# Kernel tuning notes

Hardware: AMD Instinct MI355X
Metric: run time of the kernel (lower is better)

## Reference

```python
import jax, jax.numpy as jnp
import numpy as np
from jax import lax

STRIDE = 2
PADDING = 2
KSIZE = 5


def _maxpool3d(y, k):
    # valid max pool with kernel=stride=k over the 3 spatial dims of NCDHW
    return lax.reduce_window(
        y, -jnp.inf, lax.max,
        window_dimensions=(1, 1, k, k, k),
        window_strides=(1, 1, k, k, k),
        padding='VALID')


def setup_inputs() -> dict:
    key = jax.random.key(0)
    k1, k2, k3 = jax.random.split(key, 3)
    x = jax.random.normal(k1, (16, 32, 16, 32, 32), dtype=jnp.float32)
    # torch ConvTranspose3d weight layout: (in_ch, out_ch, kD, kH, kW)
    weight = jax.random.normal(k2, (32, 64, KSIZE, KSIZE, KSIZE), dtype=jnp.float32) * 0.05
    bias = jax.random.normal(k3, (64,), dtype=jnp.float32) * 0.05
    return {"x": x, "weight": weight, "bias": bias}


def reference(x, weight, bias):
    # Fused ConvTranspose3d + sum over output channels.
    # sum_c convT(x, W)[:, c] == convT(x, W.sum(out_ch)) + bias.sum(), so we
    # pre-reduce the weight over the out-channel axis (axis=1) -- same math,
    # and it never materializes the (N, out_ch, D', H', W') intermediate,
    # exactly like the fused CUDA kernel.
    w_sum = weight.sum(axis=1)  # (in_ch, kD, kH, kW)
    # transposed conv == conv with lhs_dilation=stride, pad k-1-p, flipped kernel
    wk = w_sum[None, :, ::-1, ::-1, ::-1]  # (1, in_ch, kD, kH, kW), OIDHW
    pad = KSIZE - 1 - PADDING
    y = lax.conv_general_dilated(
        x, wk,
        window_strides=(1, 1, 1),
        padding=[(pad, pad)] * 3,
        lhs_dilation=(STRIDE, STRIDE, STRIDE),
        dimension_numbers=('NCDHW', 'OIDHW', 'NCDHW'))  # (N,1,31,63,63)
    y = y + bias.sum()
    # MaxPool3d(kernel=2) then MaxPool3d(kernel=3) on the single-channel map
    y = _maxpool3d(y, 2)  # (N,1,15,31,31)
    y = _maxpool3d(y, 3)  # (N,1,5,10,10)
    return y
```

## Files before the change

### kernel.cpp

```cpp
#include <hip/hip_runtime.h>


typedef short v8s __attribute__((ext_vector_type(8)));
typedef float v4f __attribute__((ext_vector_type(4)));
typedef unsigned short ushort_t;

#define DIN 16
#define HIN 32
#define WIN 32
#define CHSTR (DIN*HIN*WIN)
#define NSTRIDE (32*CHSTR)
#define Y_N 108000
#define Y_TOT (16*Y_N)
#define XSTR 24

#define XT_US 10653696u
#define XTN   665856u
#define PLANE_US 36992u
#define ROW_US 1088u
#define BT_BYTE_OFF 21307392u
#define WSF_BYTE_OFF 21335040u
#define NEED_MFMA (21335040u + 4097u*4u)

static __device__ __forceinline__ ushort_t f2bf(float f) {
  unsigned u = __builtin_bit_cast(unsigned, f);
  unsigned r = (u + 0x7FFFu + ((u >> 16) & 1u)) >> 16;
  return (ushort_t)r;
}

__global__ __launch_bounds__(256) void transpose_x(const float* __restrict__ x,
                                                   const float* __restrict__ w,
                                                   const float* __restrict__ bias,
                                                   ushort_t* __restrict__ xT,
                                                   ushort_t* __restrict__ Btab,
                                                   float* __restrict__ wsf) {
  int blk = blockIdx.x;
  int t = threadIdx.x;

  if (blk >= 1088) {
    int abc = blk - 1088;
    int a = abc / 9, b = (abc / 3) % 3, c = abc % 3;
    int half = t & 3;
    int l = t >> 2;
    int tt = l & 15, g = l >> 4;
    float v0 = 0.f, v1 = 0.f;
    if (tt < 8) {
      int td = tt & 1, th = (tt >> 1) & 1, tw = tt >> 2;
      int kd = td + 2 * a, kh = th + 2 * b, kw = tw + 2 * c;
      if (kd < 5 && kh < 5 && kw < 5) {
        int off = kd * 25 + kh * 5 + kw;
        const float* wp0 = w + (size_t)(8 * g + 2 * half) * 64 * 125 + off;
        const float* wp1 = wp0 + 64 * 125;
        float s0 = 0.f, s1 = 0.f;
#pragma unroll
        for (int oc = 0; oc < 64; ++oc) { s0 += wp0[oc * 125]; s1 += wp1[oc * 125]; }
        v0 = s0; v1 = s1;
      }
    }
    unsigned pk = (unsigned)f2bf(v0) | ((unsigned)f2bf(v1) << 16);
    ((unsigned*)Btab)[(abc * 64 + l) * 4 + half] = pk;
    if (abc == 0 && t == 0) {
      float bsum = 0.f;
      for (int o = 0; o < 64; ++o) bsum += bias[o];
      wsf[4096] = bsum;
    }
    return;
  }

  int hq = blk & 3;
  int dpad = (blk >> 2) % 17;
  int n = blk / 68;
  int h0 = 8 * hq;
  ushort_t* plane = xT + (size_t)(n * 18 + dpad) * PLANE_US;
  int d = dpad - 1;

  if (d < 0) {
    for (int r = 0; r < 8; ++r) {
      char* row = (char*)(plane + (size_t)(h0 + r) * ROW_US);
      for (int s = t; s < 136; s += 256)
        *(uint4*)(row + s * 16) = make_uint4(0, 0, 0, 0);
    }
    return;
  }

  __shared__ float lb[2][32 * 33];
  const float* xb = x + ((size_t)n * 32 * 16 + d) * 1024;
  int ic = t >> 3, wq = t & 7;

  {
    int h = h0 - 1;
    if (h >= 0) {
      float4 v = *(const float4*)&xb[(size_t)ic * 16384 + h * 32 + wq * 4];
      float* L = lb[0] + ic * 33 + wq * 4;
      L[0] = v.x; L[1] = v.y; L[2] = v.z; L[3] = v.w;
    }
  }
  int pp = 0;
  for (int i = 0; i < 8; ++i) {
    __syncthreads();
    if (i + 1 < 8) {
      int h = h0 + i;
      if (h <= 31) {
        float4 v = *(const float4*)&xb[(size_t)ic * 16384 + h * 32 + wq * 4];
        float* L = lb[pp ^ 1] + ic * 33 + wq * 4;
        L[0] = v.x; L[1] = v.y; L[2] = v.z; L[3] = v.w;
      }
    }
    int h = h0 + i - 1;
    ushort_t* row = plane + (size_t)(h0 + i) * ROW_US;
    bool hv = (h >= 0 && h <= 31);
    for (int s = t; s < 136; s += 256) {
      int wslot = s >> 2, q4 = s & 3;
      ushort_t o[8];
#pragma unroll
      for (int j = 0; j < 8; ++j) o[j] = 0;
      if (wslot >= 1 && wslot <= 32 && hv) {
        int w2 = wslot - 1;
        const float* L = lb[pp];
#pragma unroll
        for (int j = 0; j < 8; ++j) o[j] = f2bf(L[(8 * q4 + j) * 33 + w2]);
      }
      uint4 pk;
      pk.x = (unsigned)o[0] | ((unsigned)o[1] << 16);
      pk.y = (unsigned)o[2] | ((unsigned)o[3] << 16);
      pk.z = (unsigned)o[4] | ((unsigned)o[5] << 16);
      pk.w = (unsigned)o[6] | ((unsigned)o[7] << 16);
      *(uint4*)(row + wslot * 32 + q4 * 8) = pk;
    }
    pp ^= 1;
  }
}

__global__ __launch_bounds__(576, 7) void conv_mfma(const ushort_t* __restrict__ xT,
                                                    const ushort_t* __restrict__ Btab,
                                                    const float* __restrict__ wsf,
                                                    float* __restrict__ out) {
  __shared__ __align__(16) ushort_t As0[5440];
  __shared__ __align__(16) ushort_t As1[5440];
  __shared__ float ytile[6 * 6 * 64];
  __shared__ float red[64];

  int blk = blockIdx.x;
  int OH = blk % 10, OD = (blk / 10) % 5, n = blk / 50;
  int t = threadIdx.x;

  int wv = t >> 6, l = t & 63;
  int mdl = wv / 3, mhl = wv % 3;
  int tt = l & 15, g = l >> 4;
  const ushort_t* xn = xT + (size_t)n * XTN;
  const ushort_t* slab0 = xn + ((size_t)(3 * OD) * 34 + 3 * OH) * ROW_US;

  {
    uint4 v0 = *(const uint4*)(slab0 + t * 8);
    uint4 v1;
    if (t < 104) v1 = *(const uint4*)(slab0 + (t + 576) * 8);
    *(uint4*)&As0[t * 8] = v0;
    if (t < 104) *(uint4*)&As0[(t + 576) * 8] = v1;
  }
  __syncthreads();

  v4f acc0 = {0.f, 0.f, 0.f, 0.f};
  v4f acc1 = {0.f, 0.f, 0.f, 0.f};
  int lane_off = tt * 32 + g * 8;

  for (int p = 0; p < 5; ++p) {
    uint4 v0, v1;
    if (p < 4) {
      const ushort_t* slab = slab0 + (size_t)(p + 1) * 34 * ROW_US;
      v0 = *(const uint4*)(slab + t * 8);
      if (t < 104) v1 = *(const uint4*)(slab + (t + 576) * 8);
    }

    int a = mdl + 2 - p;
    if (0 <= a && a <= 2) {
      const ushort_t* Ab = (p & 1) ? As1 : As0;
      const ushort_t* Bg = Btab + ((size_t)a * 9 * 64 + l) * 8;
#pragma unroll
      for (int b = 0; b < 3; ++b) {
#pragma unroll
        for (int c = 0; c < 3; ++c) {
          int idx = ((mhl + 2 - b) * 34 + (2 - c)) * 32 + lane_off;
          v8s bv = *(const v8s*)(Bg + (b * 3 + c) * 512);
          v8s a0 = *(const v8s*)&Ab[idx];
          v8s a1 = *(const v8s*)&Ab[idx + 512];
          acc0 = __builtin_amdgcn_mfma_f32_16x16x32_bf16(a0, bv, acc0, 0, 0, 0);
          acc1 = __builtin_amdgcn_mfma_f32_16x16x32_bf16(a1, bv, acc1, 0, 0, 0);
        }
      }
    }

    if (p < 4) {
      ushort_t* dst = (p & 1) ? As0 : As1;
      *(uint4*)&dst[t * 8] = v0;
      if (t < 104) *(uint4*)&dst[(t + 576) * 8] = v1;
      __syncthreads();
    }
  }

  __syncthreads();
  if (tt < 8) {
    int td = tt & 1, th = (tt >> 1) & 1, tw = tt >> 2;
    int odl = 2 * mdl + td, ohl = 2 * mhl + th;
#pragma unroll
    for (int i = 0; i < 4; ++i) {
      int mwD0 = 4 * g + i;
      ytile[(odl * 6 + ohl) * 64 + 2 * mwD0 + tw] = acc0[i];
      ytile[(odl * 6 + ohl) * 64 + 2 * (16 + mwD0) + tw] = acc1[i];
    }
  }
  __syncthreads();

  if (t < 60) {
    int odl = t / 10, OW = t % 10;
    float m = -3.4e38f;
    for (int oh = 0; oh < 6; ++oh)
#pragma unroll
      for (int j = 0; j < 6; ++j)
        m = fmaxf(m, ytile[(odl * 6 + oh) * 64 + 6 * OW + j]);
    red[t] = m;
  }
  __syncthreads();
  if (t < 10) {
    float m = red[t];
#pragma unroll
    for (int odl = 1; odl < 6; ++odl) m = fmaxf(m, red[odl * 10 + t]);
    out[((n * 5 + OD) * 10 + OH) * 10 + t] = m + wsf[4096];
  }
}

template<int NCHUNK>
__global__ __launch_bounds__(256, 4) void conv_stage1(const float* __restrict__ x,
                                                      const float* __restrict__ ws,
                                                      float* part, int woff) {
  constexpr int ICPB = 32 / NCHUNK;
  constexpr int NPHS = ICPB / 2;
  __shared__ __align__(16) float xs[170 * XSTR];
  int blk = blockIdx.x;
  int s0 = blk % 320;
  int chunk = blk / 320;
  int wq = s0 & 1, hq = (s0 >> 1) & 1, dc = (s0 >> 2) % 5, n = s0 / 20;
  int t = threadIdx.x;
  int mw = t % 15, lmh = t / 15;
  int id_base = 3 * dc - 1, ih_base = 15 * hq - 1;
  int iwb = wq ? 12 : -4;
  int cb = mw + (wq ? 2 : 3);
  const float* xn = x + (size_t)n * NSTRIDE + (size_t)(chunk * ICPB) * CHSTR;
  const float* wsw = ws + woff + (size_t)(chunk * ICPB) * 128;
  float acc[3][2][2][2] = {{{{0.f}}}};
  for (int phs = 0; phs < NPHS; ++phs) {
    for (int s = t; s < 1700; s += 256) {
      int c2 = s % 10, row = s / 10;
      int bh = row % 17, q = row / 17;
      int ad = q % 5, lic = q / 5;
      int id = id_base + ad, ih = ih_base + bh, iw = iwb + 2 * c2;
      float2 v = make_float2(0.f, 0.f);
      if ((id | ih | iw) >= 0)
        v = *(const float2*)&xn[(size_t)(phs * 2 + lic) * CHSTR + (id * HIN + ih) * WIN + iw];
      *(float2*)&xs[row * XSTR + 2 * c2] = v;
    }
    __syncthreads();
    if (t < 225) {
#pragma unroll
      for (int lic = 0; lic < 2; ++lic) {
        const float* wc = wsw + (size_t)(phs * 2 + lic) * 128;
        const float* xc = &xs[(lic * 85 + lmh) * XSTR + cb];
        float xv[5][3][3];
#pragma unroll
        for (int a = 0; a < 5; ++a)
#pragma unroll
          for (int b = 0; b < 3; ++b) {
            const float* xr = xc + (a * 17 + b) * XSTR;
            xv[a][b][0] = xr[0]; xv[a][b][1] = xr[1]; xv[a][b][2] = xr[2];
          }
#pragma unroll
        for (int kd = 0; kd < 5; ++kd) {
          constexpr int DT[5] = {0, 1, 0, 1, 0};
          constexpr int AOFF[5] = {2, 2, 1, 1, 0};
          const int dt = DT[kd], aoff = AOFF[kd];
          float wv[25];
#pragma unroll
          for (int j = 0; j < 25; ++j) wv[j] = wc[kd * 25 + j];
#pragma unroll
          for (int kh = 0; kh < 5; ++kh) {
            constexpr int HT[5] = {0, 1, 0, 1, 0};
            constexpr int BOFF[5] = {2, 2, 1, 1, 0};
            const int ht = HT[kh], boff = BOFF[kh];
#pragma unroll
            for (int m = 0; m < 3; ++m) {
              const float x0 = xv[m + aoff][boff][0];
              const float x1 = xv[m + aoff][boff][1];
              const float x2 = xv[m + aoff][boff][2];
              acc[m][dt][ht][0] += x0 * wv[kh * 5 + 4];
              acc[m][dt][ht][0] += x1 * wv[kh * 5 + 2];
              acc[m][dt][ht][0] += x2 * wv[kh * 5 + 0];
              acc[m][dt][ht][1] += x1 * wv[kh * 5 + 3];
              acc[m][dt][ht][1] += x2 * wv[kh * 5 + 1];
            }
          }
        }
      }
    }
    __syncthreads();
  }
  if (t < 225) {
    float* pb = part + (size_t)chunk * Y_TOT + (size_t)n * Y_N;
#pragma unroll
    for (int m = 0; m < 3; ++m)
#pragma unroll
      for (int dt = 0; dt < 2; ++dt)
#pragma unroll
        for (int ht = 0; ht < 2; ++ht) {
          int od_g = 6 * dc + 2 * m + dt;
          int oh_g = 30 * hq + 2 * lmh + ht;
          int ow_g = 30 * wq + 2 * mw;
          *(float2*)&pb[(od_g * 60 + oh_g) * 60 + ow_g] =
              make_float2(acc[m][dt][ht][0], acc[m][dt][ht][1]);
        }
  }
}

template<int NCHUNK>
__global__ __launch_bounds__(256) void pool_stage2(const float* __restrict__ part,
                                                   const float* __restrict__ ws,
                                                   float* __restrict__ out, int woff) {
  __shared__ __align__(16) float buf[2160];
  __shared__ float red[240];
  int blk = blockIdx.x;
  int hc = blk % 10, dc = (blk / 10) % 5, n = blk / 50;
  int t = threadIdx.x;
  const float* pb = part + (size_t)n * Y_N;
  for (int s = t; s < 540; s += 256) {
    int row = s / 15, c4 = s % 15;
    int od = row / 6, oh = row % 6;
    size_t idx = (size_t)((6 * dc + od) * 60 + (6 * hc + oh)) * 60 + 4 * c4;
    float4 v = *(const float4*)&pb[idx];
#pragma unroll
    for (int c = 1; c < NCHUNK; ++c) {
      float4 u = *(const float4*)&pb[(size_t)c * Y_TOT + idx];
      v.x += u.x; v.y += u.y; v.z += u.z; v.w += u.w;
    }
    *(float4*)&buf[row * 60 + 4 * c4] = v;
  }
  __syncthreads();
  if (t < 240) {
    int wc = t / 24, sub = t % 24;
    float m = -3.4e38f;
#pragma unroll
    for (int k = 0; k < 9; ++k) {
      int e = sub + 24 * k;
      int od = e / 36, r = e % 36;
      int oh = r / 6, ow0 = r % 6;
      m = fmaxf(m, buf[(od * 6 + oh) * 60 + 6 * wc + ow0]);
    }
    red[t] = m;
  }
  __syncthreads();
  if (t < 10) {
    float mm = -3.4e38f;
#pragma unroll
    for (int s2 = 0; s2 < 24; ++s2) mm = fmaxf(mm, red[t * 24 + s2]);
    out[((n * 5 + dc) * 10 + hc) * 10 + t] = mm + ws[woff + 4096];
  }
}

__global__ __launch_bounds__(128) void prep2(const float* __restrict__ w,
                                             const float* __restrict__ bias,
                                             float* __restrict__ ws, int woff) {
  int i = blockIdx.x, t = threadIdx.x;
  if (t < 125) {
    const float* wp = w + (size_t)i * 64 * 125 + t;
    float v = 0.f;
#pragma unroll
    for (int o = 0; o < 64; ++o) v += wp[o * 125];
    ws[woff + i * 128 + t] = v;
  }
  if (i == 0 && t == 126) {
    float b = 0.f;
    for (int o = 0; o < 64; ++o) b += bias[o];
    ws[woff + 4096] = b;
  }
}

extern "C" void kernel_launch(void* const* d_in, const int* in_sizes, int n_in,
                              void* d_out, int out_size, void* d_ws, size_t ws_size,
                              hipStream_t stream) {
  const float* x    = (const float*)d_in[0];
  const float* w    = (const float*)d_in[1];
  const float* bias = (const float*)d_in[2];
  float* outp = (float*)d_out;

  if (ws_size >= (size_t)NEED_MFMA) {
    ushort_t* xT = (ushort_t*)d_ws;
    ushort_t* Bt = (ushort_t*)((char*)d_ws + BT_BYTE_OFF);
    float* wsf   = (float*)((char*)d_ws + WSF_BYTE_OFF);
    transpose_x<<<1088 + 27, 256, 0, stream>>>(x, w, bias, xT, Bt, wsf);
    conv_mfma<<<800, 576, 0, stream>>>(xT, Bt, wsf, outp);
    return;
  }

  float* ws = (float*)d_ws;
  const size_t need4 = ((size_t)4 * Y_TOT + 4097) * 4;
  const size_t need2 = ((size_t)2 * Y_TOT + 4097) * 4;
  const size_t need1 = ((size_t)1 * Y_TOT + 4097) * 4;
  if (ws_size >= need4) {
    int woff = 4 * Y_TOT;
    prep2<<<32, 128, 0, stream>>>(w, bias, ws, woff);
    conv_stage1<4><<<320 * 4, 256, 0, stream>>>(x, ws, ws, woff);
    pool_stage2<4><<<800, 256, 0, stream>>>(ws, ws, outp, woff);
  } else if (ws_size >= need2) {
    int woff = 2 * Y_TOT;
    prep2<<<32, 128, 0, stream>>>(w, bias, ws, woff);
    conv_stage1<2><<<320 * 2, 256, 0, stream>>>(x, ws, ws, woff);
    pool_stage2<2><<<800, 256, 0, stream>>>(ws, ws, outp, woff);
  } else if (ws_size >= need1) {
    int woff = 1 * Y_TOT;
    prep2<<<32, 128, 0, stream>>>(w, bias, ws, woff);
    conv_stage1<1><<<320 * 1, 256, 0, stream>>>(x, ws, ws, woff);
    pool_stage2<1><<<800, 256, 0, stream>>>(ws, ws, outp, woff);
  }
}
```

Before: 36.08 us.

## Fuse x transpose/bf16 conversion into MFMA conv kernel, drop intermediate xT buffer

Removes the separate transpose_x pass that wrote a padded bf16 copy of x to global memory. The conv kernel now loads fp32 x directly, converts it to bf16 and stores it into a swizzled LDS layout, with padding zeroed in-kernel. This drops a global write and read of about 21MB and shrinks the preceding launch to a small weight-prep kernel. In exchange, each block does strided fp32 gathers across channels (8 loads per thread, 32 lanes wide) and reloads halo data, which may coalesce worse. The fallback paths are also simplified to a single chunk.

Result: slower. 39.60 us (+9.8%).

```diff
diff --git a/kernel.cpp b/kernel.cpp
--- a/kernel.cpp
+++ b/kernel.cpp
@@ -5,136 +5,60 @@
 typedef float v4f __attribute__((ext_vector_type(4)));
 typedef unsigned short ushort_t;
 
-#define DIN 16
-#define HIN 32
-#define WIN 32
-#define CHSTR (DIN*HIN*WIN)
+#define CHSTR 16384
 #define NSTRIDE (32*CHSTR)
 #define Y_N 108000
 #define Y_TOT (16*Y_N)
 #define XSTR 24
 
-#define XT_US 10653696u
-#define XTN   665856u
-#define PLANE_US 36992u
-#define ROW_US 1088u
-#define BT_BYTE_OFF 21307392u
-#define WSF_BYTE_OFF 21335040u
-#define NEED_MFMA (21335040u + 4097u*4u)
+#define WSF_BYTE_OFF 27648u
+#define NEED_FUSED (27648u + 4097u*4u)
 
 static __device__ __forceinline__ ushort_t f2bf(float f) {
   unsigned u = __builtin_bit_cast(unsigned, f);
   unsigned r = (u + 0x7FFFu + ((u >> 16) & 1u)) >> 16;
   return (ushort_t)r;
 }
-
-__global__ __launch_bounds__(256) void transpose_x(const float* __restrict__ x,
-                                                   const float* __restrict__ w,
-                                                   const float* __restrict__ bias,
-                                                   ushort_t* __restrict__ xT,
-                                                   ushort_t* __restrict__ Btab,
-                                                   float* __restrict__ wsf) {
-  int blk = blockIdx.x;
+static __device__ __forceinline__ unsigned pk2(float a, float b) {
+  return (unsigned)f2bf(a) | ((unsigned)f2bf(b) << 16);
+}
+
+__global__ __launch_bounds__(256) void prep_bw(const float* __restrict__ w,
+                                               const float* __restrict__ bias,
+                                               ushort_t* __restrict__ Btab,
+                                               float* __restrict__ wsf) {
+  int abc = blockIdx.x;
+  int a = abc / 9, b = (abc / 3) % 3, c = abc % 3;
   int t = threadIdx.x;
-
-  if (blk >= 1088) {
-    int abc = blk - 1088;
-    int a = abc / 9, b = (abc / 3) % 3, c = abc % 3;
-    int half = t & 3;
-    int l = t >> 2;
-    int tt = l & 15, g = l >> 4;
-    float v0 = 0.f, v1 = 0.f;
-    if (tt < 8) {
-      int td = tt & 1, th = (tt >> 1) & 1, tw = tt >> 2;
-      int kd = td + 2 * a, kh = th + 2 * b, kw = tw + 2 * c;
-      if (kd < 5 && kh < 5 && kw < 5) {
-        int off = kd * 25 + kh * 5 + kw;
-        const float* wp0 = w + (size_t)(8 * g + 2 * half) * 64 * 125 + off;
-        const float* wp1 = wp0 + 64 * 125;
-        float s0 = 0.f, s1 = 0.f;
-#pragma unroll
-        for (int oc = 0; oc < 64; ++oc) { s0 += wp0[oc * 125]; s1 += wp1[oc * 125]; }
-        v0 = s0; v1 = s1;
-      }
-    }
-    unsigned pk = (unsigned)f2bf(v0) | ((unsigned)f2bf(v1) << 16);
-    ((unsigned*)Btab)[(abc * 64 + l) * 4 + half] = pk;
-    if (abc == 0 && t == 0) {
-      float bsum = 0.f;
-      for (int o = 0; o < 64; ++o) bsum += bias[o];
-      wsf[4096] = bsum;
-    }
-    return;
-  }
-
-  int hq = blk & 3;
-  int dpad = (blk >> 2) % 17;
-  int n = blk / 68;
-  int h0 = 8 * hq;
-  ushort_t* plane = xT + (size_t)(n * 18 + dpad) * PLANE_US;
-  int d = dpad - 1;
-
-  if (d < 0) {
-    for (int r = 0; r < 8; ++r) {
-      char* row = (char*)(plane + (size_t)(h0 + r) * ROW_US);
-      for (int s = t; s < 136; s += 256)
-        *(uint4*)(row + s * 16) = make_uint4(0, 0, 0, 0);
-    }
-    return;
-  }
-
-  __shared__ float lb[2][32 * 33];
-  const float* xb = x + ((size_t)n * 32 * 16 + d) * 1024;
-  int ic = t >> 3, wq = t & 7;
-
-  {
-    int h = h0 - 1;
-    if (h >= 0) {
-      float4 v = *(const float4*)&xb[(size_t)ic * 16384 + h * 32 + wq * 4];
-      float* L = lb[0] + ic * 33 + wq * 4;
-      L[0] = v.x; L[1] = v.y; L[2] = v.z; L[3] = v.w;
-    }
-  }
-  int pp = 0;
-  for (int i = 0; i < 8; ++i) {
-    __syncthreads();
-    if (i + 1 < 8) {
-      int h = h0 + i;
-      if (h <= 31) {
-        float4 v = *(const float4*)&xb[(size_t)ic * 16384 + h * 32 + wq * 4];
-        float* L = lb[pp ^ 1] + ic * 33 + wq * 4;
-        L[0] = v.x; L[1] = v.y; L[2] = v.z; L[3] = v.w;
-      }
-    }
-    int h = h0 + i - 1;
-    ushort_t* row = plane + (size_t)(h0 + i) * ROW_US;
-    bool hv = (h >= 0 && h <= 31);
-    for (int s = t; s < 136; s += 256) {
-      int wslot = s >> 2, q4 = s & 3;
-      ushort_t o[8];
-#pragma unroll
-      for (int j = 0; j < 8; ++j) o[j] = 0;
-      if (wslot >= 1 && wslot <= 32 && hv) {
-        int w2 = wslot - 1;
-        const float* L = lb[pp];
-#pragma unroll
-        for (int j = 0; j < 8; ++j) o[j] = f2bf(L[(8 * q4 + j) * 33 + w2]);
-      }
-      uint4 pk;
-      pk.x = (unsigned)o[0] | ((unsigned)o[1] << 16);
-      pk.y = (unsigned)o[2] | ((unsigned)o[3] << 16);
-      pk.z = (unsigned)o[4] | ((unsigned)o[5] << 16);
-      pk.w = (unsigned)o[6] | ((unsigned)o[7] << 16);
-      *(uint4*)(row + wslot * 32 + q4 * 8) = pk;
-    }
-    pp ^= 1;
-  }
-}
-
-__global__ __launch_bounds__(576, 7) void conv_mfma(const ushort_t* __restrict__ xT,
-                                                    const ushort_t* __restrict__ Btab,
-                                                    const float* __restrict__ wsf,
-                                                    float* __restrict__ out) {
+  int half = t & 3;
+  int l = t >> 2;
+  int tt = l & 15, g = l >> 4;
+  float v0 = 0.f, v1 = 0.f;
+  if (tt < 8) {
+    int td = tt & 1, th = (tt >> 1) & 1, tw = tt >> 2;
+    int kd = td + 2 * a, kh = th + 2 * b, kw = tw + 2 * c;
+    if (kd < 5 && kh < 5 && kw < 5) {
+      int off = kd * 25 + kh * 5 + kw;
+      const float* wp0 = w + (size_t)(8 * g + 2 * half) * 64 * 125 + off;
+      const float* wp1 = wp0 + 64 * 125;
+      float s0 = 0.f, s1 = 0.f;
+#pragma unroll
+      for (int oc = 0; oc < 64; ++oc) { s0 += wp0[oc * 125]; s1 += wp1[oc * 125]; }
+      v0 = s0; v1 = s1;
+    }
+  }
+  ((unsigned*)Btab)[(abc * 64 + l) * 4 + half] = (unsigned)f2bf(v0) | ((unsigned)f2bf(v1) << 16);
+  if (abc == 0 && t == 0) {
+    float bs = 0.f;
+    for (int o = 0; o < 64; ++o) bs += bias[o];
+    wsf[4096] = bs;
+  }
+}
+
+__global__ __launch_bounds__(576, 7) void conv_fused(const float* __restrict__ x,
+                                                     const ushort_t* __restrict__ Btab,
+                                                     const float* __restrict__ wsf,
+                                                     float* __restrict__ out) {
   __shared__ __align__(16) ushort_t As0[5440];
   __shared__ __align__(16) ushort_t As1[5440];
   __shared__ float ytile[6 * 6 * 64];
@@ -143,46 +67,86 @@
   int blk = blockIdx.x;
   int OH = blk % 10, OD = (blk / 10) % 5, n = blk / 50;
   int t = threadIdx.x;
-
   int wv = t >> 6, l = t & 63;
   int mdl = wv / 3, mhl = wv % 3;
   int tt = l & 15, g = l >> 4;
-  const ushort_t* xn = xT + (size_t)n * XTN;
-  const ushort_t* slab0 = xn + ((size_t)(3 * OD) * 34 + 3 * OH) * ROW_US;
+
+  int sw = l & 31, sich = l >> 5;
+  int wcol = sw + 1;
+  int r_u = wv >> 1, icg_u = wv & 1;
+  bool hz_u = (3 * OH + r_u) == 0;
+  const float* xu = x + (size_t)(n * 32 + icg_u * 16 + sich * 8) * CHSTR
+                      + (3 * OH + r_u - 1) * 32 + sw;
+  int waddr_u = ((r_u * 34 + wcol) << 5) + (((icg_u * 2 + sich) ^ (wcol & 3)) << 3);
+  const float* xu9 = x + (size_t)(n * 32 + 16 + sich * 8) * CHSTR + (3 * OH + 3) * 32 + sw;
+  int waddr_9 = ((4 * 34 + wcol) << 5) + (((2 + sich) ^ (wcol & 3)) << 3);
+
+  int oc0 = ((2 + tt) << 5) + ((g ^ ((tt + 2) & 3)) << 3);
+  int oc1 = ((1 + tt) << 5) + ((g ^ ((tt + 1) & 3)) << 3);
+  int oc2 = ((tt) << 5)     + ((g ^ (tt & 3)) << 3);
 
   {
-    uint4 v0 = *(const uint4*)(slab0 + t * 8);
-    uint4 v1;
-    if (t < 104) v1 = *(const uint4*)(slab0 + (t + 576) * 8);
-    *(uint4*)&As0[t * 8] = v0;
-    if (t < 104) *(uint4*)&As0[(t + 576) * 8] = v1;
+    float f[8];
+#pragma unroll
+    for (int j = 0; j < 8; ++j) f[j] = 0.f;
+    if (OD != 0 && !hz_u) {
+      const float* s = xu + (size_t)(3 * OD - 1) * 1024;
+#pragma unroll
+      for (int j = 0; j < 8; ++j) f[j] = s[(size_t)j * CHSTR];
+    }
+    uint4 pk;
+    pk.x = pk2(f[0], f[1]); pk.y = pk2(f[2], f[3]);
+    pk.z = pk2(f[4], f[5]); pk.w = pk2(f[6], f[7]);
+    *(uint4*)&As0[waddr_u] = pk;
+    if (wv == 8) {
+      float f9[8];
+#pragma unroll
+      for (int j = 0; j < 8; ++j) f9[j] = 0.f;
+      if (OD != 0) {
+        const float* s = xu9 + (size_t)(3 * OD - 1) * 1024;
+#pragma unroll
+        for (int j = 0; j < 8; ++j) f9[j] = s[(size_t)j * CHSTR];
+      }
+      uint4 p9;
+      p9.x = pk2(f9[0], f9[1]); p9.y = pk2(f9[2], f9[3]);
+      p9.z = pk2(f9[4], f9[5]); p9.w = pk2(f9[6], f9[7]);
+      *(uint4*)&As0[waddr_9] = p9;
+    }
+    if (t < 160) {
+      int seg = t >> 4;
+      int rr = seg >> 1, col = (seg & 1) ? 33 : 0;
+      *(unsigned*)&As0[((rr * 34 + col) << 5) + ((t & 15) << 1)] = 0u;
+    }
   }
   __syncthreads();
 
   v4f acc0 = {0.f, 0.f, 0.f, 0.f};
   v4f acc1 = {0.f, 0.f, 0.f, 0.f};
-  int lane_off = tt * 32 + g * 8;
 
   for (int p = 0; p < 5; ++p) {
-    uint4 v0, v1;
-    if (p < 4) {
-      const ushort_t* slab = slab0 + (size_t)(p + 1) * 34 * ROW_US;
-      v0 = *(const uint4*)(slab + t * 8);
-      if (t < 104) v1 = *(const uint4*)(slab + (t + 576) * 8);
+    float pf[8];
+#pragma unroll
+    for (int j = 0; j < 8; ++j) pf[j] = 0.f;
+    if (p < 4 && !hz_u) {
+      const float* s = xu + (size_t)(3 * OD + p) * 1024;
+#pragma unroll
+      for (int j = 0; j < 8; ++j) pf[j] = s[(size_t)j * CHSTR];
     }
 
     int a = mdl + 2 - p;
     if (0 <= a && a <= 2) {
       const ushort_t* Ab = (p & 1) ? As1 : As0;
-      const ushort_t* Bg = Btab + ((size_t)a * 9 * 64 + l) * 8;
+      const ushort_t* Bg = Btab + ((size_t)(a * 9) * 64 + l) * 8;
 #pragma unroll
       for (int b = 0; b < 3; ++b) {
+        int rb = (mhl + 2 - b) * 1088;
 #pragma unroll
         for (int c = 0; c < 3; ++c) {
-          int idx = ((mhl + 2 - b) * 34 + (2 - c)) * 32 + lane_off;
+          int offc = (c == 0) ? oc0 : (c == 1) ? oc1 : oc2;
           v8s bv = *(const v8s*)(Bg + (b * 3 + c) * 512);
-          v8s a0 = *(const v8s*)&Ab[idx];
-          v8s a1 = *(const v8s*)&Ab[idx + 512];
+          const ushort_t* ap = Ab + rb + offc;
+          v8s a0 = *(const v8s*)ap;
+          v8s a1 = *(const v8s*)(ap + 512);
           acc0 = __builtin_amdgcn_mfma_f32_16x16x32_bf16(a0, bv, acc0, 0, 0, 0);
           acc1 = __builtin_amdgcn_mfma_f32_16x16x32_bf16(a1, bv, acc1, 0, 0, 0);
         }
@@ -191,8 +155,25 @@
 
     if (p < 4) {
       ushort_t* dst = (p & 1) ? As0 : As1;
-      *(uint4*)&dst[t * 8] = v0;
-      if (t < 104) *(uint4*)&dst[(t + 576) * 8] = v1;
+      uint4 pk;
+      pk.x = pk2(pf[0], pf[1]); pk.y = pk2(pf[2], pf[3]);
+      pk.z = pk2(pf[4], pf[5]); pk.w = pk2(pf[6], pf[7]);
+      *(uint4*)&dst[waddr_u] = pk;
+      if (wv == 8) {
+        float f9[8];
+        const float* s = xu9 + (size_t)(3 * OD + p) * 1024;
+#pragma unroll
+        for (int j = 0; j < 8; ++j) f9[j] = s[(size_t)j * CHSTR];
+        uint4 p9;
+        p9.x = pk2(f9[0], f9[1]); p9.y = pk2(f9[2], f9[3]);
+        p9.z = pk2(f9[4], f9[5]); p9.w = pk2(f9[6], f9[7]);
+        *(uint4*)&dst[waddr_9] = p9;
+      }
+      if (p == 0 && t < 160) {
+        int seg = t >> 4;
+        int rr = seg >> 1, col = (seg & 1) ? 33 : 0;
+        *(unsigned*)&dst[((rr * 34 + col) << 5) + ((t & 15) << 1)] = 0u;
+      }
       __syncthreads();
     }
   }
@@ -228,26 +209,40 @@
   }
 }
 
-template<int NCHUNK>
+__global__ __launch_bounds__(128) void prep2(const float* __restrict__ w,
+                                             const float* __restrict__ bias,
+                                             float* __restrict__ ws, int woff) {
+  int i = blockIdx.x, t = threadIdx.x;
+  if (t < 125) {
+    const float* wp = w + (size_t)i * 64 * 125 + t;
+    float v = 0.f;
+#pragma unroll
+    for (int o = 0; o < 64; ++o) v += wp[o * 125];
+    ws[woff + i * 128 + t] = v;
+  }
+  if (i == 0 && t == 126) {
+    float b = 0.f;
+    for (int o = 0; o < 64; ++o) b += bias[o];
+    ws[woff + 4096] = b;
+  }
+}
+
 __global__ __launch_bounds__(256, 4) void conv_stage1(const float* __restrict__ x,
                                                       const float* __restrict__ ws,
                                                       float* part, int woff) {
-  constexpr int ICPB = 32 / NCHUNK;
-  constexpr int NPHS = ICPB / 2;
   __shared__ __align__(16) float xs[170 * XSTR];
   int blk = blockIdx.x;
   int s0 = blk % 320;
-  int chunk = blk / 320;
   int wq = s0 & 1, hq = (s0 >> 1) & 1, dc = (s0 >> 2) % 5, n = s0 / 20;
   int t = threadIdx.x;
   int mw = t % 15, lmh = t / 15;
   int id_base = 3 * dc - 1, ih_base = 15 * hq - 1;
   int iwb = wq ? 12 : -4;
   int cb = mw + (wq ? 2 : 3);
-  const float* xn = x + (size_t)n * NSTRIDE + (size_t)(chunk * ICPB) * CHSTR;
-  const float* wsw = ws + woff + (size_t)(chunk * ICPB) * 128;
+  const float* xn = x + (size_t)n * NSTRIDE;
+  const float* wsw = ws + woff;
   float acc[3][2][2][2] = {{{{0.f}}}};
-  for (int phs = 0; phs < NPHS; ++phs) {
+  for (int phs = 0; phs < 16; ++phs) {
     for (int s = t; s < 1700; s += 256) {
       int c2 = s % 10, row = s / 10;
       int bh = row % 17, q = row / 17;
@@ -255,7 +250,7 @@
       int id = id_base + ad, ih = ih_base + bh, iw = iwb + 2 * c2;
       float2 v = make_float2(0.f, 0.f);
       if ((id | ih | iw) >= 0)
-        v = *(const float2*)&xn[(size_t)(phs * 2 + lic) * CHSTR + (id * HIN + ih) * WIN + iw];
+        v = *(const float2*)&xn[(size_t)(phs * 2 + lic) * CHSTR + (id * 32 + ih) * 32 + iw];
       *(float2*)&xs[row * XSTR + 2 * c2] = v;
     }
     __syncthreads();
@@ -277,9 +272,9 @@
           constexpr int DT[5] = {0, 1, 0, 1, 0};
           constexpr int AOFF[5] = {2, 2, 1, 1, 0};
           const int dt = DT[kd], aoff = AOFF[kd];
-          float wv[25];
-#pragma unroll
-          for (int j = 0; j < 25; ++j) wv[j] = wc[kd * 25 + j];
+          float wvv[25];
+#pragma unroll
+          for (int j = 0; j < 25; ++j) wvv[j] = wc[kd * 25 + j];
 #pragma unroll
           for (int kh = 0; kh < 5; ++kh) {
             constexpr int HT[5] = {0, 1, 0, 1, 0};
@@ -290,11 +285,11 @@
               const float x0 = xv[m + aoff][boff][0];
               const float x1 = xv[m + aoff][boff][1];
               const float x2 = xv[m + aoff][boff][2];
-              acc[m][dt][ht][0] += x0 * wv[kh * 5 + 4];
-              acc[m][dt][ht][0] += x1 * wv[kh * 5 + 2];
-              acc[m][dt][ht][0] += x2 * wv[kh * 5 + 0];
-              acc[m][dt][ht][1] += x1 * wv[kh * 5 + 3];
-              acc[m][dt][ht][1] += x2 * wv[kh * 5 + 1];
+              acc[m][dt][ht][0] += x0 * wvv[kh * 5 + 4];
+              acc[m][dt][ht][0] += x1 * wvv[kh * 5 + 2];
+              acc[m][dt][ht][0] += x2 * wvv[kh * 5 + 0];
+              acc[m][dt][ht][1] += x1 * wvv[kh * 5 + 3];
+              acc[m][dt][ht][1] += x2 * wvv[kh * 5 + 1];
             }
           }
         }
@@ -303,7 +298,7 @@
     __syncthreads();
   }
   if (t < 225) {
-    float* pb = part + (size_t)chunk * Y_TOT + (size_t)n * Y_N;
+    float* pb = part + (size_t)n * Y_N;
 #pragma unroll
     for (int m = 0; m < 3; ++m)
 #pragma unroll
@@ -319,7 +314,6 @@
   }
 }
 
-template<int NCHUNK>
 __global__ __launch_bounds__(256) void pool_stage2(const float* __restrict__ part,
                                                    const float* __restrict__ ws,
                                                    float* __restrict__ out, int woff) {
@@ -333,13 +327,7 @@
     int row = s / 15, c4 = s % 15;
     int od = row / 6, oh = row % 6;
     size_t idx = (size_t)((6 * dc + od) * 60 + (6 * hc + oh)) * 60 + 4 * c4;
-    float4 v = *(const float4*)&pb[idx];
-#pragma unroll
-    for (int c = 1; c < NCHUNK; ++c) {
-      float4 u = *(const float4*)&pb[(size_t)c * Y_TOT + idx];
-      v.x += u.x; v.y += u.y; v.z += u.z; v.w += u.w;
-    }
-    *(float4*)&buf[row * 60 + 4 * c4] = v;
+    *(float4*)&buf[row * 60 + 4 * c4] = *(const float4*)&pb[idx];
   }
   __syncthreads();
   if (t < 240) {
@@ -360,24 +348,6 @@
 #pragma unroll
     for (int s2 = 0; s2 < 24; ++s2) mm = fmaxf(mm, red[t * 24 + s2]);
     out[((n * 5 + dc) * 10 + hc) * 10 + t] = mm + ws[woff + 4096];
-  }
-}
-
-__global__ __launch_bounds__(128) void prep2(const float* __restrict__ w,
-                                             const float* __restrict__ bias,
-                                             float* __restrict__ ws, int woff) {
-  int i = blockIdx.x, t = threadIdx.x;
-  if (t < 125) {
-    const float* wp = w + (size_t)i * 64 * 125 + t;
-    float v = 0.f;
-#pragma unroll
-    for (int o = 0; o < 64; ++o) v += wp[o * 125];
-    ws[woff + i * 128 + t] = v;
-  }
-  if (i == 0 && t == 126) {
-    float b = 0.f;
-    for (int o = 0; o < 64; ++o) b += bias[o];
-    ws[woff + 4096] = b;
   }
 }
 
@@ -389,33 +359,20 @@
   const float* bias = (const float*)d_in[2];
   float* outp = (float*)d_out;
 
-  if (ws_size >= (size_t)NEED_MFMA) {
-    ushort_t* xT = (ushort_t*)d_ws;
-    ushort_t* Bt = (ushort_t*)((char*)d_ws + BT_BYTE_OFF);
+  if (ws_size >= (size_t)NEED_FUSED) {
+    ushort_t* Bt = (ushort_t*)d_ws;
     float* wsf   = (float*)((char*)d_ws + WSF_BYTE_OFF);
-    transpose_x<<<1088 + 27, 256, 0, stream>>>(x, w, bias, xT, Bt, wsf);
-    conv_mfma<<<800, 576, 0, stream>>>(xT, Bt, wsf, outp);
+    prep_bw<<<27, 256, 0, stream>>>(w, bias, Bt, wsf);
+    conv_fused<<<800, 576, 0, stream>>>(x, Bt, wsf, outp);
     return;
   }
 
   float* ws = (float*)d_ws;
-  const size_t need4 = ((size_t)4 * Y_TOT + 4097) * 4;
-  const size_t need2 = ((size_t)2 * Y_TOT + 4097) * 4;
   const size_t need1 = ((size_t)1 * Y_TOT + 4097) * 4;
-  if (ws_size >= need4) {
-    int woff = 4 * Y_TOT;
+  if (ws_size >= need1) {
+    int woff = Y_TOT;
     prep2<<<32, 128, 0, stream>>>(w, bias, ws, woff);
-    conv_stage1<4><<<320 * 4, 256, 0, stream>>>(x, ws, ws, woff);
-    pool_stage2<4><<<800, 256, 0, stream>>>(ws, ws, outp, woff);
-  } else if (ws_size >= need2) {
-    int woff = 2 * Y_TOT;
-    prep2<<<32, 128, 0, stream>>>(w, bias, ws, woff);
-    conv_stage1<2><<<320 * 2, 256, 0, stream>>>(x, ws, ws, woff);
-    pool_stage2<2><<<800, 256, 0, stream>>>(ws, ws, outp, woff);
-  } else if (ws_size >= need1) {
-    int woff = 1 * Y_TOT;
-    prep2<<<32, 128, 0, stream>>>(w, bias, ws, woff);
-    conv_stage1<1><<<320 * 1, 256, 0, stream>>>(x, ws, ws, woff);
-    pool_stage2<1><<<800, 256, 0, stream>>>(ws, ws, outp, woff);
-  }
-}
+    conv_stage1<<<320, 256, 0, stream>>>(x, ws, ws, woff);
+    pool_stage2<<<800, 256, 0, stream>>>(ws, ws, outp, woff);
+  }
+}
```

## Double output rows per MFMA block to reuse A-fragments across kernel rows

Applied to the files above, without the earlier changes.

The MFMA conv kernel now computes two pooled output rows (OH pairs) per block, halving the grid to 400 blocks and loading a taller input slab. Each loaded A fragment is reused across several kernel-height taps and both output rows, so fewer LDS reads and slab loads are needed per MFMA. The larger shared buffer is aliased with the y tile to limit LDS use, which may cut occupancy. Fallback paths are simplified to a single-chunk variant.

Result: no change. 36.05 us (-0.1%).

```diff
diff --git a/kernel.cpp b/kernel.cpp
--- a/kernel.cpp
+++ b/kernel.cpp
@@ -5,10 +5,7 @@
 typedef float v4f __attribute__((ext_vector_type(4)));
 typedef unsigned short ushort_t;
 
-#define DIN 16
-#define HIN 32
-#define WIN 32
-#define CHSTR (DIN*HIN*WIN)
+#define CHSTR 16384
 #define NSTRIDE (32*CHSTR)
 #define Y_N 108000
 #define Y_TOT (16*Y_N)
@@ -57,8 +54,7 @@
         v0 = s0; v1 = s1;
       }
     }
-    unsigned pk = (unsigned)f2bf(v0) | ((unsigned)f2bf(v1) << 16);
-    ((unsigned*)Btab)[(abc * 64 + l) * 4 + half] = pk;
+    ((unsigned*)Btab)[(abc * 64 + l) * 4 + half] = (unsigned)f2bf(v0) | ((unsigned)f2bf(v1) << 16);
     if (abc == 0 && t == 0) {
       float bsum = 0.f;
       for (int o = 0; o < 64; ++o) bsum += bias[o];
@@ -131,60 +127,73 @@
   }
 }
 
-__global__ __launch_bounds__(576, 7) void conv_mfma(const ushort_t* __restrict__ xT,
-                                                    const ushort_t* __restrict__ Btab,
-                                                    const float* __restrict__ wsf,
-                                                    float* __restrict__ out) {
-  __shared__ __align__(16) ushort_t As0[5440];
-  __shared__ __align__(16) ushort_t As1[5440];
-  __shared__ float ytile[6 * 6 * 64];
-  __shared__ float red[64];
+__global__ __launch_bounds__(576, 7) void conv_mfma6(const ushort_t* __restrict__ xT,
+                                                     const ushort_t* __restrict__ Btab,
+                                                     const float* __restrict__ wsf,
+                                                     float* __restrict__ out) {
+  __shared__ __align__(16) char smem[35328];
+  ushort_t* As0 = (ushort_t*)smem;
+  ushort_t* As1 = (ushort_t*)(smem + 17408);
+  float* ytile  = (float*)smem;
+  float* red    = (float*)(smem + 34816);
 
   int blk = blockIdx.x;
-  int OH = blk % 10, OD = (blk / 10) % 5, n = blk / 50;
+  int OH2 = blk % 5, OD = (blk / 5) % 5, n = blk / 25;
   int t = threadIdx.x;
-
   int wv = t >> 6, l = t & 63;
-  int mdl = wv / 3, mhl = wv % 3;
+  int mdl = wv / 3, mhp = wv % 3;
   int tt = l & 15, g = l >> 4;
+
   const ushort_t* xn = xT + (size_t)n * XTN;
-  const ushort_t* slab0 = xn + ((size_t)(3 * OD) * 34 + 3 * OH) * ROW_US;
+  const ushort_t* slab0 = xn + ((size_t)(3 * OD) * 34 + 6 * OH2) * ROW_US;
 
   {
-    uint4 v0 = *(const uint4*)(slab0 + t * 8);
+    uint4 v0 = *(const uint4*)(slab0 + (size_t)t * 8);
     uint4 v1;
-    if (t < 104) v1 = *(const uint4*)(slab0 + (t + 576) * 8);
+    if (t < 512) v1 = *(const uint4*)(slab0 + (size_t)(t + 576) * 8);
     *(uint4*)&As0[t * 8] = v0;
-    if (t < 104) *(uint4*)&As0[(t + 576) * 8] = v1;
-  }
-  __syncthreads();
-
-  v4f acc0 = {0.f, 0.f, 0.f, 0.f};
-  v4f acc1 = {0.f, 0.f, 0.f, 0.f};
-  int lane_off = tt * 32 + g * 8;
+    if (t < 512) *(uint4*)&As0[(t + 576) * 8] = v1;
+  }
+  __syncthreads();
+
+  v4f acc[2][2];
+#pragma unroll
+  for (int m2 = 0; m2 < 2; ++m2)
+#pragma unroll
+    for (int wh = 0; wh < 2; ++wh) acc[m2][wh] = (v4f){0.f, 0.f, 0.f, 0.f};
+
+  int lane_base = (2 * mhp) * ROW_US + tt * 32 + g * 8;
 
   for (int p = 0; p < 5; ++p) {
     uint4 v0, v1;
     if (p < 4) {
-      const ushort_t* slab = slab0 + (size_t)(p + 1) * 34 * ROW_US;
-      v0 = *(const uint4*)(slab + t * 8);
-      if (t < 104) v1 = *(const uint4*)(slab + (t + 576) * 8);
+      const ushort_t* slab = slab0 + (size_t)(p + 1) * PLANE_US;
+      v0 = *(const uint4*)(slab + (size_t)t * 8);
+      if (t < 512) v1 = *(const uint4*)(slab + (size_t)(t + 576) * 8);
     }
 
     int a = mdl + 2 - p;
     if (0 <= a && a <= 2) {
       const ushort_t* Ab = (p & 1) ? As1 : As0;
-      const ushort_t* Bg = Btab + ((size_t)a * 9 * 64 + l) * 8;
-#pragma unroll
-      for (int b = 0; b < 3; ++b) {
-#pragma unroll
-        for (int c = 0; c < 3; ++c) {
-          int idx = ((mhl + 2 - b) * 34 + (2 - c)) * 32 + lane_off;
-          v8s bv = *(const v8s*)(Bg + (b * 3 + c) * 512);
-          v8s a0 = *(const v8s*)&Ab[idx];
-          v8s a1 = *(const v8s*)&Ab[idx + 512];
-          acc0 = __builtin_amdgcn_mfma_f32_16x16x32_bf16(a0, bv, acc0, 0, 0, 0);
-          acc1 = __builtin_amdgcn_mfma_f32_16x16x32_bf16(a1, bv, acc1, 0, 0, 0);
+      const ushort_t* Bg = Btab + ((size_t)(a * 9) * 64 + l) * 8;
+#pragma unroll
+      for (int c = 0; c < 3; ++c) {
+        v8s bv0 = *(const v8s*)(Bg + (0 * 3 + c) * 512);
+        v8s bv1 = *(const v8s*)(Bg + (1 * 3 + c) * 512);
+        v8s bv2 = *(const v8s*)(Bg + (2 * 3 + c) * 512);
+#pragma unroll
+        for (int wh = 0; wh < 2; ++wh) {
+          const ushort_t* ap = Ab + lane_base + (2 - c + 16 * wh) * 32;
+          v8s a0 = *(const v8s*)(ap);
+          v8s a1 = *(const v8s*)(ap + 1 * ROW_US);
+          v8s a2 = *(const v8s*)(ap + 2 * ROW_US);
+          v8s a3 = *(const v8s*)(ap + 3 * ROW_US);
+          acc[0][wh] = __builtin_amdgcn_mfma_f32_16x16x32_bf16(a0, bv2, acc[0][wh], 0, 0, 0);
+          acc[0][wh] = __builtin_amdgcn_mfma_f32_16x16x32_bf16(a1, bv1, acc[0][wh], 0, 0, 0);
+          acc[0][wh] = __builtin_amdgcn_mfma_f32_16x16x32_bf16(a2, bv0, acc[0][wh], 0, 0, 0);
+          acc[1][wh] = __builtin_amdgcn_mfma_f32_16x16x32_bf16(a1, bv2, acc[1][wh], 0, 0, 0);
+          acc[1][wh] = __builtin_amdgcn_mfma_f32_16x16x32_bf16(a2, bv1, acc[1][wh], 0, 0, 0);
+          acc[1][wh] = __builtin_amdgcn_mfma_f32_16x16x32_bf16(a3, bv0, acc[1][wh], 0, 0, 0);
         }
       }
     }
@@ -192,7 +201,7 @@
     if (p < 4) {
       ushort_t* dst = (p & 1) ? As0 : As1;
       *(uint4*)&dst[t * 8] = v0;
-      if (t < 104) *(uint4*)&dst[(t + 576) * 8] = v1;
+      if (t < 512) *(uint4*)&dst[(t + 576) * 8] = v1;
       __syncthreads();
     }
   }
@@ -200,54 +209,73 @@
   __syncthreads();
   if (tt < 8) {
     int td = tt & 1, th = (tt >> 1) & 1, tw = tt >> 2;
-    int odl = 2 * mdl + td, ohl = 2 * mhl + th;
-#pragma unroll
-    for (int i = 0; i < 4; ++i) {
-      int mwD0 = 4 * g + i;
-      ytile[(odl * 6 + ohl) * 64 + 2 * mwD0 + tw] = acc0[i];
-      ytile[(odl * 6 + ohl) * 64 + 2 * (16 + mwD0) + tw] = acc1[i];
-    }
-  }
-  __syncthreads();
-
-  if (t < 60) {
-    int odl = t / 10, OW = t % 10;
+    int odl = 2 * mdl + td;
+#pragma unroll
+    for (int m2 = 0; m2 < 2; ++m2) {
+      int ohl = 2 * (2 * mhp + m2) + th;
+      float* yrow = &ytile[(odl * 12 + ohl) * 64];
+#pragma unroll
+      for (int wh = 0; wh < 2; ++wh)
+#pragma unroll
+        for (int i = 0; i < 4; ++i)
+          yrow[2 * (16 * wh + 4 * g + i) + tw] = acc[m2][wh][i];
+    }
+  }
+  __syncthreads();
+
+  if (t < 120) {
+    int OW = t % 10, p_oh = (t / 10) & 1, odl = t / 20;
     float m = -3.4e38f;
     for (int oh = 0; oh < 6; ++oh)
 #pragma unroll
       for (int j = 0; j < 6; ++j)
-        m = fmaxf(m, ytile[(odl * 6 + oh) * 64 + 6 * OW + j]);
+        m = fmaxf(m, ytile[(odl * 12 + 6 * p_oh + oh) * 64 + 6 * OW + j]);
     red[t] = m;
   }
   __syncthreads();
-  if (t < 10) {
-    float m = red[t];
-#pragma unroll
-    for (int odl = 1; odl < 6; ++odl) m = fmaxf(m, red[odl * 10 + t]);
-    out[((n * 5 + OD) * 10 + OH) * 10 + t] = m + wsf[4096];
-  }
-}
-
-template<int NCHUNK>
+  if (t < 20) {
+    int OW = t % 10, p_oh = t / 10;
+    float m = red[p_oh * 10 + OW];
+#pragma unroll
+    for (int odl = 1; odl < 6; ++odl) m = fmaxf(m, red[odl * 20 + p_oh * 10 + OW]);
+    out[((n * 5 + OD) * 10 + (2 * OH2 + p_oh)) * 10 + OW] = m + wsf[4096];
+  }
+}
+
+__global__ __launch_bounds__(128) void prep2(const float* __restrict__ w,
+                                             const float* __restrict__ bias,
+                                             float* __restrict__ ws, int woff) {
+  int i = blockIdx.x, t = threadIdx.x;
+  if (t < 125) {
+    const float* wp = w + (size_t)i * 64 * 125 + t;
+    float v = 0.f;
+#pragma unroll
+    for (int o = 0; o < 64; ++o) v += wp[o * 125];
+    ws[woff + i * 128 + t] = v;
+  }
+  if (i == 0 && t == 126) {
+    float b = 0.f;
+    for (int o = 0; o < 64; ++o) b += bias[o];
+    ws[woff + 4096] = b;
+  }
+}
+
 __global__ __launch_bounds__(256, 4) void conv_stage1(const float* __restrict__ x,
                                                       const float* __restrict__ ws,
                                                       float* part, int woff) {
-  constexpr int ICPB = 32 / NCHUNK;
-  constexpr int NPHS = ICPB / 2;
   __shared__ __align__(16) float xs[170 * XSTR];
   int blk = blockIdx.x;
   int s0 = blk % 320;
-  int chunk = blk / 320;
   int wq = s0 & 1, hq = (s0 >> 1) & 1, dc = (s0 >> 2) % 5, n = s0 / 20;
   int t = threadIdx.x;
   int mw = t % 15, lmh = t / 15;
   int id_base = 3 * dc - 1, ih_base = 15 * hq - 1;
   int iwb = wq ? 12 : -4;
   int cb = mw + (wq ? 2 : 3);
-  const float* xn = x + (size_t)n * NSTRIDE + (size_t)(chunk * ICPB) * CHSTR;
-  const float* wsw = ws + woff + (size_t)(chunk * ICPB) * 128;
+  const float* xn = x + (size_t)n * NSTRIDE;
+  const float* wsw = ws + woff;
   float acc[3][2][2][2] = {{{{0.f}}}};
-  for (int phs = 0; phs < NPHS; ++phs) {
+  for (int phs = 0; phs < 16; ++phs) {
     for (int s = t; s < 1700; s += 256) {
       int c2 = s % 10, row = s / 10;
       int bh = row % 17, q = row / 17;
@@ -255,7 +283,7 @@
       int id = id_base + ad, ih = ih_base + bh, iw = iwb + 2 * c2;
       float2 v = make_float2(0.f, 0.f);
       if ((id | ih | iw) >= 0)
-        v = *(const float2*)&xn[(size_t)(phs * 2 + lic) * CHSTR + (id * HIN + ih) * WIN + iw];
+        v = *(const float2*)&xn[(size_t)(phs * 2 + lic) * CHSTR + (id * 32 + ih) * 32 + iw];
       *(float2*)&xs[row * XSTR + 2 * c2] = v;
     }
     __syncthreads();
@@ -277,9 +305,9 @@
           constexpr int DT[5] = {0, 1, 0, 1, 0};
           constexpr int AOFF[5] = {2, 2, 1, 1, 0};
           const int dt = DT[kd], aoff = AOFF[kd];
-          float wv[25];
-#pragma unroll
-          for (int j = 0; j < 25; ++j) wv[j] = wc[kd * 25 + j];
+          float wvv[25];
+#pragma unroll
+          for (int j = 0; j < 25; ++j) wvv[j] = wc[kd * 25 + j];
 #pragma unroll
           for (int kh = 0; kh < 5; ++kh) {
             constexpr int HT[5] = {0, 1, 0, 1, 0};
@@ -290,11 +318,11 @@
               const float x0 = xv[m + aoff][boff][0];
               const float x1 = xv[m + aoff][boff][1];
               const float x2 = xv[m + aoff][boff][2];
-              acc[m][dt][ht][0] += x0 * wv[kh * 5 + 4];
-              acc[m][dt][ht][0] += x1 * wv[kh * 5 + 2];
-              acc[m][dt][ht][0] += x2 * wv[kh * 5 + 0];
-              acc[m][dt][ht][1] += x1 * wv[kh * 5 + 3];
-              acc[m][dt][ht][1] += x2 * wv[kh * 5 + 1];
+              acc[m][dt][ht][0] += x0 * wvv[kh * 5 + 4];
+              acc[m][dt][ht][0] += x1 * wvv[kh * 5 + 2];
+              acc[m][dt][ht][0] += x2 * wvv[kh * 5 + 0];
+              acc[m][dt][ht][1] += x1 * wvv[kh * 5 + 3];
+              acc[m][dt][ht][1] += x2 * wvv[kh * 5 + 1];
             }
           }
         }
@@ -303,7 +331,7 @@
     __syncthreads();
   }
   if (t < 225) {
-    float* pb = part + (size_t)chunk * Y_TOT + (size_t)n * Y_N;
+    float* pb = part + (size_t)n * Y_N;
 #pragma unroll
     for (int m = 0; m < 3; ++m)
 #pragma unroll
@@ -319,7 +347,6 @@
   }
 }
 
-template<int NCHUNK>
 __global__ __launch_bounds__(256) void pool_stage2(const float* __restrict__ part,
                                                    const float* __restrict__ ws,
                                                    float* __restrict__ out, int woff) {
@@ -333,13 +360,7 @@
     int row = s / 15, c4 = s % 15;
     int od = row / 6, oh = row % 6;
     size_t idx = (size_t)((6 * dc + od) * 60 + (6 * hc + oh)) * 60 + 4 * c4;
-    float4 v = *(const float4*)&pb[idx];
-#pragma unroll
-    for (int c = 1; c < NCHUNK; ++c) {
-      float4 u = *(const float4*)&pb[(size_t)c * Y_TOT + idx];
-      v.x += u.x; v.y += u.y; v.z += u.z; v.w += u.w;
-    }
-    *(float4*)&buf[row * 60 + 4 * c4] = v;
+    *(float4*)&buf[row * 60 + 4 * c4] = *(const float4*)&pb[idx];
   }
   __syncthreads();
   if (t < 240) {
@@ -360,24 +381,6 @@
 #pragma unroll
     for (int s2 = 0; s2 < 24; ++s2) mm = fmaxf(mm, red[t * 24 + s2]);
     out[((n * 5 + dc) * 10 + hc) * 10 + t] = mm + ws[woff + 4096];
-  }
-}
-
-__global__ __launch_bounds__(128) void prep2(const float* __restrict__ w,
-                                             const float* __restrict__ bias,
-                                             float* __restrict__ ws, int woff) {
-  int i = blockIdx.x, t = threadIdx.x;
-  if (t < 125) {
-    const float* wp = w + (size_t)i * 64 * 125 + t;
-    float v = 0.f;
-#pragma unroll
-    for (int o = 0; o < 64; ++o) v += wp[o * 125];
-    ws[woff + i * 128 + t] = v;
-  }
-  if (i == 0 && t == 126) {
-    float b = 0.f;
-    for (int o = 0; o < 64; ++o) b += bias[o];
-    ws[woff + 4096] = b;
   }
 }
 
@@ -394,28 +397,16 @@
     ushort_t* Bt = (ushort_t*)((char*)d_ws + BT_BYTE_OFF);
     float* wsf   = (float*)((char*)d_ws + WSF_BYTE_OFF);
     transpose_x<<<1088 + 27, 256, 0, stream>>>(x, w, bias, xT, Bt, wsf);
-    conv_mfma<<<800, 576, 0, stream>>>(xT, Bt, wsf, outp);
+    conv_mfma6<<<400, 576, 0, stream>>>(xT, Bt, wsf, outp);
     return;
   }
 
   float* ws = (float*)d_ws;
-  const size_t need4 = ((size_t)4 * Y_TOT + 4097) * 4;
-  const size_t need2 = ((size_t)2 * Y_TOT + 4097) * 4;
   const size_t need1 = ((size_t)1 * Y_TOT + 4097) * 4;
-  if (ws_size >= need4) {
-    int woff = 4 * Y_TOT;
+  if (ws_size >= need1) {
+    int woff = Y_TOT;
     prep2<<<32, 128, 0, stream>>>(w, bias, ws, woff);
-    conv_stage1<4><<<320 * 4, 256, 0, stream>>>(x, ws, ws, woff);
-    pool_stage2<4><<<800, 256, 0, stream>>>(ws, ws, outp, woff);
-  } else if (ws_size >= need2) {
-    int woff = 2 * Y_TOT;
-    prep2<<<32, 128, 0, stream>>>(w, bias, ws, woff);
-    conv_stage1<2><<<320 * 2, 256, 0, stream>>>(x, ws, ws, woff);
-    pool_stage2<2><<<800, 256, 0, stream>>>(ws, ws, outp, woff);
-  } else if (ws_size >= need1) {
-    int woff = 1 * Y_TOT;
-    prep2<<<32, 128, 0, stream>>>(w, bias, ws, woff);
-    conv_stage1<1><<<320 * 1, 256, 0, stream>>>(x, ws, ws, woff);
-    pool_stage2<1><<<800, 256, 0, stream>>>(ws, ws, outp, woff);
-  }
-}
+    conv_stage1<<<320, 256, 0, stream>>>(x, ws, ws, woff);
+    pool_stage2<<<800, 256, 0, stream>>>(ws, ws, outp, woff);
+  }
+}
```
